# Kernel optimization log

Hardware: AMD Instinct MI355X
Metric: run time of the kernel (lower is better)

The kernel has to match this reference:

```python
import jax, jax.numpy as jnp
import numpy as np

ALG_DIM = 248   # dim of E8 adjoint rep
NNZ = 30000     # number of nonzero structure constants f_{ij}^k
BATCH = 8192


def setup_inputs() -> dict:
    key = jax.random.key(0)
    k1, k2, k3, k4, k5, k6 = jax.random.split(key, 6)
    x = jax.random.normal(k1, (BATCH, ALG_DIM), dtype=jnp.float32)
    y = jax.random.normal(k2, (BATCH, ALG_DIM), dtype=jnp.float32)
    idx_i = jax.random.randint(k3, (NNZ,), 0, ALG_DIM, dtype=jnp.int32)
    idx_j = jax.random.randint(k4, (NNZ,), 0, ALG_DIM, dtype=jnp.int32)
    idx_k = jax.random.randint(k5, (NNZ,), 0, ALG_DIM, dtype=jnp.int32)
    coeff = jax.random.normal(k6, (NNZ,), dtype=jnp.float32)
    alpha = jnp.ones((1,), dtype=jnp.float32)
    return {"x": x, "y": y, "idx_i": idx_i, "idx_j": idx_j,
            "idx_k": idx_k, "coeff": coeff, "alpha": alpha}


def reference(x, y, idx_i, idx_j, idx_k, coeff, alpha):
    # Sparse Lie bracket via structure-constant triples:
    #   out[b, k] = sum_{t : idx_k[t]==k} coeff[t] * x[b, idx_i[t]] * y[b, idx_j[t]]
    vals = x[:, idx_i] * y[:, idx_j] * coeff[None, :]          # (B, nnz)
    bracket = jnp.zeros_like(x).at[:, idx_k].add(vals)          # (B, 248)
    return alpha[0] * bracket
```

## Files before the change

### kernel.cpp

```cpp
#include <hip/hip_runtime.h>

#define ALG_DIM 248
#define ROWS 32
#define KSPLIT 4
#define KPB 62
#define CAP 256
#define CNT_STRIDE 16
#define PLSTRIDE_B 3984
#define PLSTRIDE_DW 996

typedef __fp16 h2v __attribute__((ext_vector_type(2)));
union H2U { unsigned u; h2v h; };


__global__ void k_scatter(const int* __restrict__ idx_i, const int* __restrict__ idx_j,
                          const int* __restrict__ idx_k, const float* __restrict__ coeff,
                          int* __restrict__ cnt, uint2* __restrict__ packed, int nnz) {
    const int t = blockIdx.x * 256 + threadIdx.x;
    if (t >= nnz) return;
    const int k = idx_k[t];
    const int pos = atomicAdd(&cnt[k * CNT_STRIDE], 1);
    if (pos < CAP - 8) {
        const float c = coeff[t];
        H2U hc; hc.h = __builtin_amdgcn_cvt_pkrtz(c, c);
        uint2 p;
        p.x = ((unsigned)idx_i[t] << 4) | ((unsigned)idx_j[t] << 20);
        p.y = hc.u;
        packed[((size_t)k << 8) + pos] = p;
    }
}


__global__ __launch_bounds__(256, 4) void k_main(
    const float* __restrict__ x, const float* __restrict__ y,
    const uint4* __restrict__ packed4,
    const int* __restrict__ cnt,
    const float* __restrict__ alpha_p, float* __restrict__ out)
{
    __shared__ __align__(16) unsigned xs32[4 * PLSTRIDE_DW];
    __shared__ __align__(16) unsigned ys32[4 * PLSTRIDE_DW];

    const int tid = threadIdx.x;
    const int r0  = blockIdx.x * ROWS;

    for (int u = tid; u < (ALG_DIM / 4) * (ROWS / 2); u += 256) {
        const int rp = u & 15;
        const int cq = u >> 4;
        const size_t ra = (size_t)(r0 + 2 * rp) * ALG_DIM + 4 * cq;
        const float4 xa = *reinterpret_cast<const float4*>(x + ra);
        const float4 xb = *reinterpret_cast<const float4*>(x + ra + ALG_DIM);
        const float4 ya = *reinterpret_cast<const float4*>(y + ra);
        const float4 yb = *reinterpret_cast<const float4*>(y + ra + ALG_DIM);
        const int pbase = (rp >> 2) * PLSTRIDE_DW + (rp & 3);
#define STG(d, XA, XB, YA, YB)                                                  \
        {                                                                       \
            const int dw = pbase + (4 * cq + (d)) * 4;                          \
            H2U hx; hx.h = __builtin_amdgcn_cvt_pkrtz(XA, XB);                  \
            H2U hy; hy.h = __builtin_amdgcn_cvt_pkrtz(YA, YB);                  \
            xs32[dw] = hx.u;                                                    \
            ys32[dw] = hy.u;                                                    \
        }
        STG(0, xa.x, xb.x, ya.x, yb.x)
        STG(1, xa.y, xb.y, ya.y, yb.y)
        STG(2, xa.z, xb.z, ya.z, yb.z)
        STG(3, xa.w, xb.w, ya.w, yb.w)
#undef STG
    }
    __syncthreads();

    const float alpha = alpha_p[0];
    const int   S     = tid >> 2;
    const int   q     = tid & 3;

    const char* xsb = reinterpret_cast<const char*>(xs32) + q * PLSTRIDE_B;
    const char* ysb = reinterpret_cast<const char*>(ys32) + q * PLSTRIDE_B;

    const int p   = blockIdx.y * KPB + S;
    int msz = (S < KPB) ? cnt[p * CNT_STRIDE] : 0;
    int m = msz;
    m = max(m, __shfl_xor(m, 4));
    m = max(m, __shfl_xor(m, 8));
    m = max(m, __shfl_xor(m, 16));
    m = max(m, __shfl_xor(m, 32));
    const int trip = __builtin_amdgcn_readfirstlane((m + 7) & ~7);
    const int nH   = trip >> 1;

    if (S < KPB) {
        const int k = p;
        const uint4* tp = packed4 + ((size_t)p << 7);

        float a0 = 0.f, a1 = 0.f, a2 = 0.f, a3 = 0.f,
              a4 = 0.f, a5 = 0.f, a6 = 0.f, a7 = 0.f;

        uint4 cur = tp[0];

#define PROC(PW, PC)                                                            \
        {                                                                       \
            const unsigned ox = (PW) & 0xFFFFu;                                 \
            const unsigned oy = (PW) >> 16;                                     \
            const uint4 wx = *reinterpret_cast<const uint4*>(xsb + ox);         \
            const uint4 wy = *reinterpret_cast<const uint4*>(ysb + oy);         \
            H2U cc; cc.u = (PC);                                                \
            H2U ux, uy;                                                         \
            ux.u = wx.x; uy.u = wy.x; c0 = (ux.h * uy.h) * cc.h + c0;           \
            ux.u = wx.y; uy.u = wy.y; c1 = (ux.h * uy.h) * cc.h + c1;           \
            ux.u = wx.z; uy.u = wy.z; c2 = (ux.h * uy.h) * cc.h + c2;           \
            ux.u = wx.w; uy.u = wy.w; c3 = (ux.h * uy.h) * cc.h + c3;           \
        }

        for (int chunk = 0; chunk < nH; chunk += 16) {
            h2v c0 = (h2v)0.0f, c1 = (h2v)0.0f, c2 = (h2v)0.0f, c3 = (h2v)0.0f;
            const int hend = min(chunk + 16, nH);
#pragma unroll 2
            for (int h = chunk; h < hend; ++h) {
                const uint4 nxt = tp[h + 1];
                PROC(cur.x, cur.y)
                PROC(cur.z, cur.w)
                cur = nxt;
            }
            a0 += (float)c0.x; a1 += (float)c0.y;
            a2 += (float)c1.x; a3 += (float)c1.y;
            a4 += (float)c2.x; a5 += (float)c2.y;
            a6 += (float)c3.x; a7 += (float)c3.y;
        }
#undef PROC

        const int rbase = r0 + (q << 3);
        out[(size_t)(rbase + 0) * ALG_DIM + k] = alpha * a0;
        out[(size_t)(rbase + 1) * ALG_DIM + k] = alpha * a1;
        out[(size_t)(rbase + 2) * ALG_DIM + k] = alpha * a2;
        out[(size_t)(rbase + 3) * ALG_DIM + k] = alpha * a3;
        out[(size_t)(rbase + 4) * ALG_DIM + k] = alpha * a4;
        out[(size_t)(rbase + 5) * ALG_DIM + k] = alpha * a5;
        out[(size_t)(rbase + 6) * ALG_DIM + k] = alpha * a6;
        out[(size_t)(rbase + 7) * ALG_DIM + k] = alpha * a7;
    }
}


extern "C" void kernel_launch(void* const* d_in, const int* in_sizes, int n_in,
                              void* d_out, int out_size, void* d_ws, size_t ws_size,
                              hipStream_t stream) {
    const float* x      = (const float*)d_in[0];
    const float* y      = (const float*)d_in[1];
    const int*   idx_i  = (const int*)d_in[2];
    const int*   idx_j  = (const int*)d_in[3];
    const int*   idx_k  = (const int*)d_in[4];
    const float* coeff  = (const float*)d_in[5];
    const float* alpha  = (const float*)d_in[6];
    float*       out    = (float*)d_out;

    const int nnz   = in_sizes[2];
    const int batch = in_sizes[0] / ALG_DIM;

    char*  ws     = (char*)d_ws;
    int*   cnt    = (int*)ws;
    uint2* packed = (uint2*)(ws + 16384);

    const size_t zbytes = 16384 + (size_t)ALG_DIM * CAP * sizeof(uint2);
    hipMemsetAsync(ws, 0, zbytes, stream);

    k_scatter<<<(nnz + 255) / 256, 256, 0, stream>>>(idx_i, idx_j, idx_k, coeff,
                                                     cnt, packed, nnz);

    dim3 grid(batch / ROWS, KSPLIT);
    k_main<<<grid, 256, 0, stream>>>(x, y, (const uint4*)packed, cnt, alpha, out);
}
```

Measured before the change: 108.2 us.

## Replace memset and global-atomic scatter with owner-computes bucket kernel

```diff
diff --git a/kernel.cpp b/kernel.cpp
--- a/kernel.cpp
+++ b/kernel.cpp
@@ -13,21 +13,42 @@
 union H2U { unsigned u; h2v h; };
 
 
-__global__ void k_scatter(const int* __restrict__ idx_i, const int* __restrict__ idx_j,
-                          const int* __restrict__ idx_k, const float* __restrict__ coeff,
-                          int* __restrict__ cnt, uint2* __restrict__ packed, int nnz) {
-    const int t = blockIdx.x * 256 + threadIdx.x;
-    if (t >= nnz) return;
-    const int k = idx_k[t];
-    const int pos = atomicAdd(&cnt[k * CNT_STRIDE], 1);
-    if (pos < CAP - 8) {
-        const float c = coeff[t];
-        H2U hc; hc.h = __builtin_amdgcn_cvt_pkrtz(c, c);
-        uint2 p;
-        p.x = ((unsigned)idx_i[t] << 4) | ((unsigned)idx_j[t] << 20);
-        p.y = hc.u;
-        packed[((size_t)k << 8) + pos] = p;
+__global__ __launch_bounds__(256) void k_scatter_own(
+    const int* __restrict__ idx_i, const int* __restrict__ idx_j,
+    const int* __restrict__ idx_k, const float* __restrict__ coeff,
+    int* __restrict__ cnt, uint2* __restrict__ packed, int nnz)
+{
+    __shared__ int lcnt[4];
+    const int tid = threadIdx.x;
+    const int bx  = blockIdx.x;
+    const int kb  = bx << 2;
+
+    if (tid < 4) lcnt[tid] = 0;
+    __syncthreads();
+
+    for (int t = tid; t < nnz; t += 256) {
+        const int k = idx_k[t];
+        if ((k >> 2) == bx) {
+            const int pos = atomicAdd(&lcnt[k & 3], 1);
+            if (pos < CAP) {
+                const float c = coeff[t];
+                H2U hc; hc.h = __builtin_amdgcn_cvt_pkrtz(c, c);
+                uint2 p;
+                p.x = ((unsigned)idx_i[t] << 4) | ((unsigned)idx_j[t] << 20);
+                p.y = hc.u;
+                packed[((size_t)k << 8) + pos] = p;
+            }
+        }
     }
+    __syncthreads();
+
+    for (int b = 0; b < 4; ++b) {
+        const int k  = kb + b;
+        const int sz = min(lcnt[b], CAP);
+        for (int e = sz + tid; e < CAP; e += 256)
+            packed[((size_t)k << 8) + e] = make_uint2(0u, 0u);
+    }
+    if (tid < 4) cnt[(kb + tid) * CNT_STRIDE] = lcnt[tid];
 }
 
 
@@ -76,13 +97,12 @@
     const char* ysb = reinterpret_cast<const char*>(ys32) + q * PLSTRIDE_B;
 
     const int p   = blockIdx.y * KPB + S;
-    int msz = (S < KPB) ? cnt[p * CNT_STRIDE] : 0;
-    int m = msz;
+    int m = (S < KPB) ? cnt[p * CNT_STRIDE] : 0;
     m = max(m, __shfl_xor(m, 4));
     m = max(m, __shfl_xor(m, 8));
     m = max(m, __shfl_xor(m, 16));
     m = max(m, __shfl_xor(m, 32));
-    const int trip = __builtin_amdgcn_readfirstlane((m + 7) & ~7);
+    const int trip = __builtin_amdgcn_readfirstlane(min((m + 7) & ~7, CAP - 8));
     const int nH   = trip >> 1;
 
     if (S < KPB) {
@@ -157,11 +177,8 @@
     int*   cnt    = (int*)ws;
     uint2* packed = (uint2*)(ws + 16384);
 
-    const size_t zbytes = 16384 + (size_t)ALG_DIM * CAP * sizeof(uint2);
-    hipMemsetAsync(ws, 0, zbytes, stream);
-
-    k_scatter<<<(nnz + 255) / 256, 256, 0, stream>>>(idx_i, idx_j, idx_k, coeff,
-                                                     cnt, packed, nnz);
+    k_scatter_own<<<KPB, 256, 0, stream>>>(idx_i, idx_j, idx_k, coeff,
+                                           cnt, packed, nnz);
 
     dim3 grid(batch / ROWS, KSPLIT);
     k_main<<<grid, 256, 0, stream>>>(x, y, (const uint4*)packed, cnt, alpha, out);
```

Measured after the change: 150.5 us. 1.39x slower.
